# Performance work log

Hardware: AMD Instinct MI355X
Metric: run time of the kernel (lower is better)

Reference implementation:

```python
import jax, jax.numpy as jnp
import numpy as np

EPS = 1e-6  # flax GroupNorm default


def group_norm(x, scale, bias, num_groups):
    B, H, W, C = x.shape
    xg = x.reshape(B, H, W, num_groups, C // num_groups)
    mean = jnp.mean(xg, axis=(1, 2, 4), keepdims=True)
    var = jnp.var(xg, axis=(1, 2, 4), keepdims=True)
    xg = (xg - mean) * jax.lax.rsqrt(var + EPS)
    return xg.reshape(B, H, W, C) * scale + bias


def nin(h, w, b):
    # 1x1 conv / per-pixel dense: bhwc,cd->bhwd
    return jnp.einsum('bhwc,cd->bhwd', h, w) + b


def setup_inputs() -> dict:
    key = jax.random.key(0)
    ks = jax.random.split(key, 8)
    B, H, W, C = 16, 64, 64, 128
    s = 1.0 / np.sqrt(C)
    return {
        'x': jax.random.normal(ks[0], (B, H, W, C), jnp.float32),
        'gn_scale': jnp.ones((C,), jnp.float32),
        'gn_bias': jnp.zeros((C,), jnp.float32),
        'wq': jax.random.normal(ks[1], (C, C), jnp.float32) * s,
        'bq': jnp.zeros((C,), jnp.float32),
        'wk': jax.random.normal(ks[2], (C, C), jnp.float32) * s,
        'bk': jnp.zeros((C,), jnp.float32),
        'wv': jax.random.normal(ks[3], (C, C), jnp.float32) * s,
        'bv': jnp.zeros((C,), jnp.float32),
        'wo': jax.random.normal(ks[4], (C, C), jnp.float32) * s,
        'bo': jnp.zeros((C,), jnp.float32),
    }


def reference(x, gn_scale, gn_bias, wq, bq, wk, bk, wv, bv, wo, bo):
    B, H, W, C = x.shape
    num_groups = min(C // 4, 32)
    h = group_norm(x, gn_scale, gn_bias, num_groups)
    q = nin(h, wq, bq)
    k = nin(h, wk, bk)
    v = nin(h, wv, bv)
    # dense spatial attention; logits (B,H,W,H*W) materialized as in original
    w = jnp.einsum('bhwc,bHWc->bhwHW', q, k) * (C ** -0.5)
    w = w.reshape(B, H, W, H * W)
    w = jax.nn.softmax(w, axis=-1)
    w = w.reshape(B, H, W, H, W)
    h = jnp.einsum('bhwHW,bHWc->bhwc', w, v)
    h = nin(h, wo, bo)
    return x + h  # skip_rescale=False
```

## Files before the change

kernel.cpp:

```cpp
#include <hip/hip_runtime.h>
#include <hip/hip_bf16.h>

typedef unsigned short ushort_t;
typedef unsigned int uint_t;
typedef __attribute__((ext_vector_type(8))) short bf16x8;
typedef __attribute__((ext_vector_type(4))) float f32x4;

#define MFMA32(a, b, c) __builtin_amdgcn_mfma_f32_16x16x32_bf16(a, b, c, 0, 0, 0)

static constexpr int BATCH = 16;
static constexpr int SEQ   = 4096;
static constexpr int CH    = 128;
static constexpr int NGRP  = 32;
static constexpr float EPS = 1e-6f;
static constexpr float C2 = 0.08838834764831845f * 1.4426950408889634f;

__device__ inline ushort_t f2bf(float f) {
    uint_t u = __float_as_uint(f);
    u = (u + 0x7fff + ((u >> 16) & 1)) >> 16;
    return (ushort_t)u;
}

__device__ inline float exp2_fast(float x) {
    return __builtin_amdgcn_exp2f(x);
}

__global__ void gn_partial(const float* __restrict__ x, float* __restrict__ stats) {
    int bid = blockIdx.x;
    int b = bid >> 4, chunk = bid & 15;
    int t = threadIdx.x;
    int c4 = (t & 31) * 4;
    int rowoff = t >> 5;
    const float* xb = x + (size_t)b * SEQ * CH;
    float s1 = 0.f, s2 = 0.f;
    int base_row = chunk * 256;
    for (int i = 0; i < 32; ++i) {
        int r = base_row + i * 8 + rowoff;
        float4 v = *(const float4*)(xb + (size_t)r * CH + c4);
        s1 += v.x + v.y + v.z + v.w;
        s2 += v.x * v.x + v.y * v.y + v.z * v.z + v.w * v.w;
    }
    __shared__ float red[256][2];
    red[t][0] = s1; red[t][1] = s2;
    __syncthreads();
    if (t < 32) {
        float a1 = 0.f, a2 = 0.f;
        for (int ro = 0; ro < 8; ++ro) {
            a1 += red[ro * 32 + t][0];
            a2 += red[ro * 32 + t][1];
        }
        atomicAdd(&stats[(b * NGRP + t) * 2 + 0], a1);
        atomicAdd(&stats[(b * NGRP + t) * 2 + 1], a2);
    }
}

__global__ __launch_bounds__(256) void gemm_qkv(const float* __restrict__ x,
                                                const float* __restrict__ stats,
                                                const float* __restrict__ gsc,
                                                const float* __restrict__ gbi,
                                                const float* __restrict__ Wq,
                                                const float* __restrict__ Wk,
                                                const float* __restrict__ Wv,
                                                const float* __restrict__ Bq,
                                                const float* __restrict__ Bk,
                                                const float* __restrict__ Bv,
                                                ushort_t* __restrict__ outq,
                                                ushort_t* __restrict__ outk,
                                                ushort_t* __restrict__ outvt) {
    __shared__ ushort_t lds_a[128][136];
    __shared__ ushort_t lds_w[128][72];
    __shared__ float2 gstat[32];
    int t = threadIdx.x;
    int wv = t >> 6, lane = t & 63, quad = lane >> 4, l16 = lane & 15;
    size_t m0 = (size_t)blockIdx.x * 128;
    int batch = (int)(m0 >> 12);
    int seq0  = (int)(m0 & 4095);
    if (t < 32) {
        float sum = stats[(batch * NGRP + t) * 2 + 0];
        float sq  = stats[(batch * NGRP + t) * 2 + 1];
        float mean = sum / 16384.f;
        float var  = sq / 16384.f - mean * mean;
        gstat[t] = float2{mean, __frsqrt_rn(var + EPS)};
    }
    __syncthreads();
    for (int i = 0; i < 8; ++i) {
        int idx = (t + i * 256) * 8;
        int r = idx >> 7, c = idx & 127;
        size_t row = m0 + r;
        float4 xa = *(const float4*)(x + row * CH + c);
        float4 xc = *(const float4*)(x + row * CH + c + 4);
        float2 stA = gstat[c >> 2];
        float2 stB = gstat[(c >> 2) + 1];
        float4 sA = *(const float4*)(gsc + c), sB = *(const float4*)(gsc + c + 4);
        float4 bA = *(const float4*)(gbi + c), bB = *(const float4*)(gbi + c + 4);
        ushort_t tmp[8];
        tmp[0] = f2bf((xa.x - stA.x) * stA.y * sA.x + bA.x);
        tmp[1] = f2bf((xa.y - stA.x) * stA.y * sA.y + bA.y);
        tmp[2] = f2bf((xa.z - stA.x) * stA.y * sA.z + bA.z);
        tmp[3] = f2bf((xa.w - stA.x) * stA.y * sA.w + bA.w);
        tmp[4] = f2bf((xc.x - stB.x) * stB.y * sB.x + bB.x);
        tmp[5] = f2bf((xc.y - stB.x) * stB.y * sB.y + bB.y);
        tmp[6] = f2bf((xc.z - stB.x) * stB.y * sB.z + bB.z);
        tmp[7] = f2bf((xc.w - stB.x) * stB.y * sB.w + bB.w);
        *(uint4*)&lds_a[r][c] = *(const uint4*)tmp;
    }
    for (int j = 0; j < 3; ++j) {
        const float* W  = (j == 0) ? Wq : (j == 1) ? Wk : Wv;
        const float* Bi = (j == 0) ? Bq : (j == 1) ? Bk : Bv;
        f32x4 acc[2][8] = {};
        for (int kh = 0; kh < 2; ++kh) {
            int k0 = kh * 64;
            __syncthreads();
            for (int i = 0; i < 8; ++i) {
                int idx = (t + i * 256) * 4;
                int kl = idx >> 7, n = idx & 127;
                float4 wf = *(const float4*)(W + (size_t)(k0 + kl) * CH + n);
                lds_w[n + 0][kl] = f2bf(wf.x);
                lds_w[n + 1][kl] = f2bf(wf.y);
                lds_w[n + 2][kl] = f2bf(wf.z);
                lds_w[n + 3][kl] = f2bf(wf.w);
            }
            __syncthreads();
            for (int ks = 0; ks < 2; ++ks) {
                bf16x8 afrag[2];
                for (int tr = 0; tr < 2; ++tr)
                    afrag[tr] = *(const bf16x8*)&lds_a[wv * 32 + tr * 16 + l16][k0 + ks * 32 + quad * 8];
                for (int tc = 0; tc < 8; ++tc) {
                    bf16x8 bfrag = *(const bf16x8*)&lds_w[tc * 16 + l16][ks * 32 + quad * 8];
                    for (int tr = 0; tr < 2; ++tr)
                        acc[tr][tc] = MFMA32(afrag[tr], bfrag, acc[tr][tc]);
                }
            }
        }
        for (int tc = 0; tc < 8; ++tc) {
            int col = tc * 16 + l16;
            float bval = Bi[col];
            for (int tr = 0; tr < 2; ++tr) {
                int rl = wv * 32 + tr * 16 + quad * 4;
                for (int r = 0; r < 4; ++r) {
                    float vv = acc[tr][tc][r] + bval;
                    if (j == 0) vv *= C2;
                    if (j == 2) {
                        outvt[(size_t)batch * CH * SEQ + (size_t)col * SEQ + seq0 + rl + r] = f2bf(vv);
                    } else {
                        ushort_t* op = (j == 0) ? outq : outk;
                        op[(m0 + rl + r) * CH + col] = f2bf(vv);
                    }
                }
            }
        }
    }
}

__global__ __launch_bounds__(256, 2) void flash_attn18(const ushort_t* __restrict__ q,
                                                       const ushort_t* __restrict__ k,
                                                       const ushort_t* __restrict__ vt,
                                                       ushort_t* __restrict__ o) {
    int bid = blockIdx.x;
    int b = bid & 15, qt = bid >> 4;
    int t = threadIdx.x;
    int wv = t >> 6, lane = t & 63, quad = lane >> 4, l16 = lane & 15;
    const size_t SB = (size_t)SEQ * CH;
    const ushort_t* qb  = q  + (size_t)b * SB;
    const ushort_t* kb  = k  + (size_t)b * SB;
    const ushort_t* vtb = vt + (size_t)b * SB;

    __shared__ ushort_t lds_k[2][64][136];
    __shared__ ushort_t lds_vt[2][128][72];

    int qrow_base = qt * 128 + wv * 32;
    bf16x8 qfrag[2][4];
#pragma unroll
    for (int nt = 0; nt < 2; ++nt)
#pragma unroll
        for (int ks = 0; ks < 4; ++ks)
            qfrag[nt][ks] = *(const bf16x8*)(qb + (size_t)(qrow_base + nt * 16 + l16) * CH + ks * 32 + quad * 8);

    f32x4 oacc[8][2] = {};
    float psum[2] = {0.f, 0.f};

    int kr_row  = t >> 4;
    int kr_col  = (t & 15) * 8;
    int vr_d    = t >> 3;
    int vr_beta = t & 7;
    int vc0 = 32 * (vr_beta >> 2) + 16 * (vr_beta & 1) + 4 * ((vr_beta >> 1) & 1);

    const ushort_t* kp = kb + (size_t)kr_row * CH + kr_col;
    const ushort_t* vp = vtb + (size_t)vr_d * SEQ + vr_beta * 8;

    uint4 kr[4], vr[4], k1[4];
#pragma unroll
    for (int i = 0; i < 4; ++i) kr[i] = *(const uint4*)(kp + (size_t)i * 16 * CH);
#pragma unroll
    for (int i = 0; i < 4; ++i) vr[i] = *(const uint4*)(vp + (size_t)i * 32 * SEQ);
#pragma unroll
    for (int i = 0; i < 4; ++i) k1[i] = *(const uint4*)(kp + (size_t)(64 + i * 16) * CH);
    kp += 2 * 64 * CH;
    vp += 64;
#pragma unroll
    for (int i = 0; i < 4; ++i) {
        *(uint4*)&lds_k[0][kr_row + 16 * i][kr_col] = kr[i];
        *(uint4*)&lds_k[1][kr_row + 16 * i][kr_col] = k1[i];
        *(uint2*)&lds_vt[0][vr_d + 32 * i][vc0]     = uint2{vr[i].x, vr[i].y};
        *(uint2*)&lds_vt[0][vr_d + 32 * i][vc0 + 8] = uint2{vr[i].z, vr[i].w};
    }
    __syncthreads();

    bf16x8 pkp[2][2];
    {
        f32x4 s[4][2] = {};
#pragma unroll
        for (int ks = 0; ks < 4; ++ks) {
            bf16x8 kf[4];
#pragma unroll
            for (int kt = 0; kt < 4; ++kt)
                kf[kt] = *(const bf16x8*)&lds_k[0][kt * 16 + l16][ks * 32 + quad * 8];
#pragma unroll
            for (int kt = 0; kt < 4; ++kt) {
                s[kt][0] = MFMA32(kf[kt], qfrag[0][ks], s[kt][0]);
                s[kt][1] = MFMA32(kf[kt], qfrag[1][ks], s[kt][1]);
            }
        }
#pragma unroll
        for (int nt = 0; nt < 2; ++nt) {
            float ps = 0.f;
            uint_t pb[8];
#pragma unroll
            for (int kt = 0; kt < 4; ++kt) {
                float p0 = exp2_fast(s[kt][nt][0]);
                float p1 = exp2_fast(s[kt][nt][1]);
                float p2 = exp2_fast(s[kt][nt][2]);
                float p3 = exp2_fast(s[kt][nt][3]);
                ps += (p0 + p1) + (p2 + p3);
                __hip_bfloat162 h01 = __float22bfloat162_rn(float2{p0, p1});
                __hip_bfloat162 h23 = __float22bfloat162_rn(float2{p2, p3});
                __builtin_memcpy(&pb[kt * 2 + 0], &h01, 4);
                __builtin_memcpy(&pb[kt * 2 + 1], &h23, 4);
            }
            psum[nt] += ps;
            __builtin_memcpy(&pkp[nt][0], &pb[0], 16);
            __builtin_memcpy(&pkp[nt][1], &pb[4], 16);
        }
    }
    __syncthreads();

    for (int it = 0; it < 63; ++it) {
        int knxt = (it + 1) & 1;
        int vcur = it & 1;
#pragma unroll
        for (int i = 0; i < 4; ++i) kr[i] = *(const uint4*)(kp + (size_t)i * 16 * CH);
#pragma unroll
        for (int i = 0; i < 4; ++i) vr[i] = *(const uint4*)(vp + (size_t)i * 32 * SEQ);
        kp += 64 * CH; vp += 64;

        f32x4 s[4][2] = {};
#pragma unroll
        for (int u = 0; u < 4; ++u) {
            bf16x8 kf[4];
#pragma unroll
            for (int kt = 0; kt < 4; ++kt)
                kf[kt] = *(const bf16x8*)&lds_k[knxt][kt * 16 + l16][u * 32 + quad * 8];
#pragma unroll
            for (int kt = 0; kt < 4; ++kt) {
                s[kt][0] = MFMA32(kf[kt], qfrag[0][u], s[kt][0]);
                s[kt][1] = MFMA32(kf[kt], qfrag[1][u], s[kt][1]);
            }
#pragma unroll
            for (int m2 = 0; m2 < 2; ++m2) {
                int mt = u * 2 + m2;
                bf16x8 vf0 = *(const bf16x8*)&lds_vt[vcur][mt * 16 + l16][quad * 8];
                bf16x8 vf1 = *(const bf16x8*)&lds_vt[vcur][mt * 16 + l16][32 + quad * 8];
                oacc[mt][0] = MFMA32(vf0, pkp[0][0], oacc[mt][0]);
                oacc[mt][0] = MFMA32(vf1, pkp[0][1], oacc[mt][0]);
                oacc[mt][1] = MFMA32(vf0, pkp[1][0], oacc[mt][1]);
                oacc[mt][1] = MFMA32(vf1, pkp[1][1], oacc[mt][1]);
            }
        }

#pragma unroll
        for (int nt = 0; nt < 2; ++nt) {
            float ps = 0.f;
            uint_t pb[8];
#pragma unroll
            for (int kt = 0; kt < 4; ++kt) {
                float p0 = exp2_fast(s[kt][nt][0]);
                float p1 = exp2_fast(s[kt][nt][1]);
                float p2 = exp2_fast(s[kt][nt][2]);
                float p3 = exp2_fast(s[kt][nt][3]);
                ps += (p0 + p1) + (p2 + p3);
                __hip_bfloat162 h01 = __float22bfloat162_rn(float2{p0, p1});
                __hip_bfloat162 h23 = __float22bfloat162_rn(float2{p2, p3});
                __builtin_memcpy(&pb[kt * 2 + 0], &h01, 4);
                __builtin_memcpy(&pb[kt * 2 + 1], &h23, 4);
            }
            psum[nt] += ps;
            __builtin_memcpy(&pkp[nt][0], &pb[0], 16);
            __builtin_memcpy(&pkp[nt][1], &pb[4], 16);
        }

#pragma unroll
        for (int i = 0; i < 4; ++i) {
            *(uint4*)&lds_k[vcur][kr_row + 16 * i][kr_col] = kr[i];
            *(uint2*)&lds_vt[knxt][vr_d + 32 * i][vc0]     = uint2{vr[i].x, vr[i].y};
            *(uint2*)&lds_vt[knxt][vr_d + 32 * i][vc0 + 8] = uint2{vr[i].z, vr[i].w};
        }
        __syncthreads();
    }

#pragma unroll
    for (int mt = 0; mt < 8; ++mt) {
        bf16x8 vf0 = *(const bf16x8*)&lds_vt[1][mt * 16 + l16][quad * 8];
        bf16x8 vf1 = *(const bf16x8*)&lds_vt[1][mt * 16 + l16][32 + quad * 8];
        oacc[mt][0] = MFMA32(vf0, pkp[0][0], oacc[mt][0]);
        oacc[mt][0] = MFMA32(vf1, pkp[0][1], oacc[mt][0]);
        oacc[mt][1] = MFMA32(vf0, pkp[1][0], oacc[mt][1]);
        oacc[mt][1] = MFMA32(vf1, pkp[1][1], oacc[mt][1]);
    }

#pragma unroll
    for (int nt = 0; nt < 2; ++nt) {
        float tot = psum[nt];
        tot += __shfl_xor(tot, 16, 64);
        tot += __shfl_xor(tot, 32, 64);
        float inv = 1.f / tot;
        size_t row = (size_t)b * SEQ + qrow_base + nt * 16 + l16;
#pragma unroll
        for (int mt = 0; mt < 8; ++mt) {
            ushort_t tmp[4];
#pragma unroll
            for (int r = 0; r < 4; ++r) tmp[r] = f2bf(oacc[mt][nt][r] * inv);
            *(uint2*)&o[row * CH + mt * 16 + quad * 4] = *(const uint2*)tmp;
        }
    }
}

__global__ __launch_bounds__(256) void gemm_out(const ushort_t* __restrict__ A,
                                                const float* __restrict__ W,
                                                const float* __restrict__ bias,
                                                const float* __restrict__ resid,
                                                float* __restrict__ out) {
    __shared__ ushort_t lds_a[128][72];
    __shared__ ushort_t lds_w[128][72];
    int t = threadIdx.x;
    int wv = t >> 6, lane = t & 63, quad = lane >> 4, l16 = lane & 15;
    size_t m0 = (size_t)blockIdx.x * 128;
    f32x4 acc[2][8] = {};
    for (int kh = 0; kh < 2; ++kh) {
        int k0 = kh * 64;
        __syncthreads();
        for (int i = 0; i < 4; ++i) {
            int idx = (t + i * 256) * 8;
            int r = idx >> 6, c = idx & 63;
            *(uint4*)&lds_a[r][c] = *(const uint4*)(A + (m0 + r) * CH + k0 + c);
        }
        for (int i = 0; i < 8; ++i) {
            int idx = (t + i * 256) * 4;
            int kl = idx >> 7, n = idx & 127;
            float4 wf = *(const float4*)(W + (size_t)(k0 + kl) * CH + n);
            lds_w[n + 0][kl] = f2bf(wf.x);
            lds_w[n + 1][kl] = f2bf(wf.y);
            lds_w[n + 2][kl] = f2bf(wf.z);
            lds_w[n + 3][kl] = f2bf(wf.w);
        }
        __syncthreads();
        for (int ks = 0; ks < 2; ++ks) {
            bf16x8 afrag[2];
            for (int tr = 0; tr < 2; ++tr)
                afrag[tr] = *(const bf16x8*)&lds_a[wv * 32 + tr * 16 + l16][ks * 32 + quad * 8];
            for (int tc = 0; tc < 8; ++tc) {
                bf16x8 bfrag = *(const bf16x8*)&lds_w[tc * 16 + l16][ks * 32 + quad * 8];
                for (int tr = 0; tr < 2; ++tr)
                    acc[tr][tc] = MFMA32(afrag[tr], bfrag, acc[tr][tc]);
            }
        }
    }
    for (int tc = 0; tc < 8; ++tc) {
        int col = tc * 16 + l16;
        float bval = bias[col];
        for (int tr = 0; tr < 2; ++tr) {
            int rl = wv * 32 + tr * 16 + quad * 4;
            for (int r = 0; r < 4; ++r) {
                size_t row = m0 + rl + r;
                out[row * CH + col] = acc[tr][tc][r] + bval + resid[row * CH + col];
            }
        }
    }
}

extern "C" void kernel_launch(void* const* d_in, const int* in_sizes, int n_in,
                              void* d_out, int out_size, void* d_ws, size_t ws_size,
                              hipStream_t stream) {
    const float* x   = (const float*)d_in[0];
    const float* gsc = (const float*)d_in[1];
    const float* gbi = (const float*)d_in[2];
    const float* wq  = (const float*)d_in[3];
    const float* bq  = (const float*)d_in[4];
    const float* wk  = (const float*)d_in[5];
    const float* bk  = (const float*)d_in[6];
    const float* wvp = (const float*)d_in[7];
    const float* bv  = (const float*)d_in[8];
    const float* wo  = (const float*)d_in[9];
    const float* bo  = (const float*)d_in[10];
    float* outp = (float*)d_out;

    const size_t NELEM = (size_t)BATCH * SEQ * CH;
    float*    stats = (float*)d_ws;
    ushort_t* qbuf  = (ushort_t*)((char*)d_ws + 4096);
    ushort_t* kbuf  = qbuf + NELEM;
    ushort_t* vtbuf = kbuf + NELEM;
    ushort_t* abuf  = vtbuf + NELEM;

    hipMemsetAsync(stats, 0, BATCH * NGRP * 2 * sizeof(float), stream);
    gn_partial<<<256, 256, 0, stream>>>(x, stats);
    gemm_qkv<<<512, 256, 0, stream>>>(x, stats, gsc, gbi, wq, wk, wvp, bq, bk, bv,
                                      qbuf, kbuf, vtbuf);
    flash_attn18<<<512, 256, 0, stream>>>(qbuf, kbuf, vtbuf, abuf);
    gemm_out<<<512, 256, 0, stream>>>(abuf, wo, bo, x, outp);
}
```

Before: 299.9 us.

## Pre-transpose weights to bf16 once and read B fragments from global memory

Adds a small kernel that converts and transposes all four weight matrices to bf16 once per call. The QKV and output GEMMs then load B fragments directly from that buffer through global/L2 instead of having every block redo the fp32-to-bf16 transpose into LDS, which also drops several barriers. The V-transpose store is vectorized to 4-element writes, and gemm_out now stages the full A tile once. The trade-off is more global-memory fragment loads per MFMA, which rely on L2 hits, plus one extra kernel launch. These GEMMs are a small share of total time next to flash attention.

```diff
diff --git a/kernel.cpp b/kernel.cpp
--- a/kernel.cpp
+++ b/kernel.cpp
@@ -23,6 +23,35 @@
 
 __device__ inline float exp2_fast(float x) {
     return __builtin_amdgcn_exp2f(x);
+}
+
+__global__ __launch_bounds__(256) void wprep(const float* __restrict__ W0,
+                                             const float* __restrict__ W1,
+                                             const float* __restrict__ W2,
+                                             const float* __restrict__ W3,
+                                             ushort_t* __restrict__ wt) {
+    const float* Ws[4] = {W0, W1, W2, W3};
+    const float* W = Ws[blockIdx.x];
+    ushort_t* out = wt + (size_t)blockIdx.x * CH * CH;
+    __shared__ ushort_t tile[128][130];
+    int t = threadIdx.x;
+    for (int i = 0; i < 16; ++i) {
+        int idx = (t + i * 256) * 4;
+        int kk = idx >> 7, n = idx & 127;
+        float4 w4 = *(const float4*)(W + (size_t)kk * CH + n);
+        tile[n + 0][kk] = f2bf(w4.x);
+        tile[n + 1][kk] = f2bf(w4.y);
+        tile[n + 2][kk] = f2bf(w4.z);
+        tile[n + 3][kk] = f2bf(w4.w);
+    }
+    __syncthreads();
+    for (int i = 0; i < 8; ++i) {
+        int idx = (t + i * 256) * 8;
+        int n = idx >> 7, kk = idx & 127;
+        ushort_t tmp[8];
+        for (int u = 0; u < 8; ++u) tmp[u] = tile[n][kk + u];
+        *(uint4*)&out[(size_t)n * CH + kk] = *(const uint4*)tmp;
+    }
 }
 
 __global__ void gn_partial(const float* __restrict__ x, float* __restrict__ stats) {
@@ -58,9 +87,7 @@
                                                 const float* __restrict__ stats,
                                                 const float* __restrict__ gsc,
                                                 const float* __restrict__ gbi,
-                                                const float* __restrict__ Wq,
-                                                const float* __restrict__ Wk,
-                                                const float* __restrict__ Wv,
+                                                const ushort_t* __restrict__ wt,
                                                 const float* __restrict__ Bq,
                                                 const float* __restrict__ Bk,
                                                 const float* __restrict__ Bv,
@@ -68,7 +95,6 @@
                                                 ushort_t* __restrict__ outk,
                                                 ushort_t* __restrict__ outvt) {
     __shared__ ushort_t lds_a[128][136];
-    __shared__ ushort_t lds_w[128][72];
     __shared__ float2 gstat[32];
     int t = threadIdx.x;
     int wv = t >> 6, lane = t & 63, quad = lane >> 4, l16 = lane & 15;
@@ -104,29 +130,19 @@
         tmp[7] = f2bf((xc.w - stB.x) * stB.y * sB.w + bB.w);
         *(uint4*)&lds_a[r][c] = *(const uint4*)tmp;
     }
+    __syncthreads();
     for (int j = 0; j < 3; ++j) {
-        const float* W  = (j == 0) ? Wq : (j == 1) ? Wk : Wv;
+        const ushort_t* wtj = wt + (size_t)j * CH * CH;
         const float* Bi = (j == 0) ? Bq : (j == 1) ? Bk : Bv;
         f32x4 acc[2][8] = {};
         for (int kh = 0; kh < 2; ++kh) {
             int k0 = kh * 64;
-            __syncthreads();
-            for (int i = 0; i < 8; ++i) {
-                int idx = (t + i * 256) * 4;
-                int kl = idx >> 7, n = idx & 127;
-                float4 wf = *(const float4*)(W + (size_t)(k0 + kl) * CH + n);
-                lds_w[n + 0][kl] = f2bf(wf.x);
-                lds_w[n + 1][kl] = f2bf(wf.y);
-                lds_w[n + 2][kl] = f2bf(wf.z);
-                lds_w[n + 3][kl] = f2bf(wf.w);
-            }
-            __syncthreads();
             for (int ks = 0; ks < 2; ++ks) {
                 bf16x8 afrag[2];
                 for (int tr = 0; tr < 2; ++tr)
                     afrag[tr] = *(const bf16x8*)&lds_a[wv * 32 + tr * 16 + l16][k0 + ks * 32 + quad * 8];
                 for (int tc = 0; tc < 8; ++tc) {
-                    bf16x8 bfrag = *(const bf16x8*)&lds_w[tc * 16 + l16][ks * 32 + quad * 8];
+                    bf16x8 bfrag = *(const bf16x8*)(wtj + (size_t)(tc * 16 + l16) * CH + k0 + ks * 32 + quad * 8);
                     for (int tr = 0; tr < 2; ++tr)
                         acc[tr][tc] = MFMA32(afrag[tr], bfrag, acc[tr][tc]);
                 }
@@ -137,13 +153,16 @@
             float bval = Bi[col];
             for (int tr = 0; tr < 2; ++tr) {
                 int rl = wv * 32 + tr * 16 + quad * 4;
-                for (int r = 0; r < 4; ++r) {
-                    float vv = acc[tr][tc][r] + bval;
-                    if (j == 0) vv *= C2;
-                    if (j == 2) {
-                        outvt[(size_t)batch * CH * SEQ + (size_t)col * SEQ + seq0 + rl + r] = f2bf(vv);
-                    } else {
-                        ushort_t* op = (j == 0) ? outq : outk;
+                if (j == 2) {
+                    ushort_t tmp[4];
+                    for (int r = 0; r < 4; ++r) tmp[r] = f2bf(acc[tr][tc][r] + bval);
+                    *(uint2*)&outvt[(size_t)batch * CH * SEQ + (size_t)col * SEQ + seq0 + rl] =
+                        *(const uint2*)tmp;
+                } else {
+                    ushort_t* op = (j == 0) ? outq : outk;
+                    for (int r = 0; r < 4; ++r) {
+                        float vv = acc[tr][tc][r] + bval;
+                        if (j == 0) vv *= C2;
                         op[(m0 + rl + r) * CH + col] = f2bf(vv);
                     }
                 }
@@ -335,40 +354,29 @@
 }
 
 __global__ __launch_bounds__(256) void gemm_out(const ushort_t* __restrict__ A,
-                                                const float* __restrict__ W,
+                                                const ushort_t* __restrict__ wto,
                                                 const float* __restrict__ bias,
                                                 const float* __restrict__ resid,
                                                 float* __restrict__ out) {
-    __shared__ ushort_t lds_a[128][72];
-    __shared__ ushort_t lds_w[128][72];
+    __shared__ ushort_t lds_a[128][136];
     int t = threadIdx.x;
     int wv = t >> 6, lane = t & 63, quad = lane >> 4, l16 = lane & 15;
     size_t m0 = (size_t)blockIdx.x * 128;
+    for (int i = 0; i < 8; ++i) {
+        int idx = (t + i * 256) * 8;
+        int r = idx >> 7, c = idx & 127;
+        *(uint4*)&lds_a[r][c] = *(const uint4*)(A + (m0 + r) * CH + c);
+    }
+    __syncthreads();
     f32x4 acc[2][8] = {};
     for (int kh = 0; kh < 2; ++kh) {
         int k0 = kh * 64;
-        __syncthreads();
-        for (int i = 0; i < 4; ++i) {
-            int idx = (t + i * 256) * 8;
-            int r = idx >> 6, c = idx & 63;
-            *(uint4*)&lds_a[r][c] = *(const uint4*)(A + (m0 + r) * CH + k0 + c);
-        }
-        for (int i = 0; i < 8; ++i) {
-            int idx = (t + i * 256) * 4;
-            int kl = idx >> 7, n = idx & 127;
-            float4 wf = *(const float4*)(W + (size_t)(k0 + kl) * CH + n);
-            lds_w[n + 0][kl] = f2bf(wf.x);
-            lds_w[n + 1][kl] = f2bf(wf.y);
-            lds_w[n + 2][kl] = f2bf(wf.z);
-            lds_w[n + 3][kl] = f2bf(wf.w);
-        }
-        __syncthreads();
         for (int ks = 0; ks < 2; ++ks) {
             bf16x8 afrag[2];
             for (int tr = 0; tr < 2; ++tr)
-                afrag[tr] = *(const bf16x8*)&lds_a[wv * 32 + tr * 16 + l16][ks * 32 + quad * 8];
+                afrag[tr] = *(const bf16x8*)&lds_a[wv * 32 + tr * 16 + l16][k0 + ks * 32 + quad * 8];
             for (int tc = 0; tc < 8; ++tc) {
-                bf16x8 bfrag = *(const bf16x8*)&lds_w[tc * 16 + l16][ks * 32 + quad * 8];
+                bf16x8 bfrag = *(const bf16x8*)(wto + (size_t)(tc * 16 + l16) * CH + k0 + ks * 32 + quad * 8);
                 for (int tr = 0; tr < 2; ++tr)
                     acc[tr][tc] = MFMA32(afrag[tr], bfrag, acc[tr][tc]);
             }
@@ -409,11 +417,13 @@
     ushort_t* kbuf  = qbuf + NELEM;
     ushort_t* vtbuf = kbuf + NELEM;
     ushort_t* abuf  = vtbuf + NELEM;
+    ushort_t* wtbuf = abuf + NELEM;
 
     hipMemsetAsync(stats, 0, BATCH * NGRP * 2 * sizeof(float), stream);
+    wprep<<<4, 256, 0, stream>>>(wq, wk, wvp, wo, wtbuf);
     gn_partial<<<256, 256, 0, stream>>>(x, stats);
-    gemm_qkv<<<512, 256, 0, stream>>>(x, stats, gsc, gbi, wq, wk, wvp, bq, bk, bv,
+    gemm_qkv<<<512, 256, 0, stream>>>(x, stats, gsc, gbi, wtbuf, bq, bk, bv,
                                       qbuf, kbuf, vtbuf);
-    flash_attn18<<<512, 256, 0, stream>>>(qbuf, kbuf, vtbuf, abuf);
-    gemm_out<<<512, 256, 0, stream>>>(abuf, wo, bo, x, outp);
-}
+    flash_attn18<<<512, 512 / 2, 0, stream>>>(qbuf, kbuf, vtbuf, abuf);
+    gemm_out<<<512, 256, 0, stream>>>(abuf, wtbuf + 3 * CH * CH, bo, x, outp);
+}
```

New measurement: 293.4 us. 2.1% less time.
